# Kernel tuning notes

Measured on AMD Instinct MI355X. Metric: run time of the kernel, lower is better.

Reference implementation:

```python
import jax, jax.numpy as jnp
import numpy as np


def setup_inputs() -> dict:
    key = jax.random.key(0)
    x = jax.random.normal(key, (4, 512, 64, 64), dtype=jnp.float32)
    return {"x": x}


def reference(x) -> jnp.ndarray:
    B, C, H, W = x.shape
    N = H * W
    v = x.reshape(B, C, N)                      # proj_query/key/value all = x flattened
    # energy[b, i, j] = sum_c x[b,c,i] * x[b,c,j]
    energy = jnp.einsum('bci,bcj->bij', v, v)
    attention = jax.nn.softmax(energy, axis=-1)  # softmax over last dim (keys j)
    # out[b,c,i] = sum_j v[b,c,j] * attention[b,i,j]  (== V @ attention^T)
    out = jnp.einsum('bcj,bij->bci', v, attention)
    return out.reshape(B, C, H, W)
```

## Files before the change

kernel.cpp:

```cpp
#include <hip/hip_runtime.h>
#include <hip/hip_bf16.h>

typedef unsigned short u16;
typedef unsigned int   u32;
typedef unsigned long long u64;
typedef __attribute__((ext_vector_type(8))) short bf16x8;
typedef __attribute__((ext_vector_type(4))) float f32x4;

#define BB 4
#define CC 512
#define NN 4096
#define LOG2E 1.44269504f

static __device__ __forceinline__ u16 f2b(float f) {
    __hip_bfloat16 h = __float2bfloat16(f);
    return *(u16*)&h;
}
static __device__ __forceinline__ u16 f2b_fast(float f) {
    u32 u = __builtin_bit_cast(u32, f);
    return (u16)((u + 0x8000u) >> 16);
}
static __device__ __forceinline__ float b2f(u16 b) {
    u32 u = (u32)b << 16;
    return __builtin_bit_cast(float, u);
}

typedef __attribute__((address_space(1))) const u32 GU32;
typedef __attribute__((address_space(3))) u32 LU32;
__device__ __forceinline__ void async16(const void* g, void* l) {
    __builtin_amdgcn_global_load_lds((GU32*)g, (LU32*)l, 16, 0, 0);
}

__global__ __launch_bounds__(256) void prep_kernel(const float* __restrict__ x,
                                                   u16* __restrict__ XT,
                                                   u16* __restrict__ XN,
                                                   float* __restrict__ normp) {
    __shared__ __align__(8) u16 tile[64][68];
    __shared__ float nsum[64];
    int blk = blockIdx.x;
    int b  = blk >> 9;
    int r2 = blk & 511;
    int cg = r2 >> 6;
    int c0 = cg << 6;
    int n0 = (r2 & 63) << 6;
    int t  = threadIdx.x;
    if (t < 64) nsum[t] = 0.f;

    int nq    = t & 15;
    int rbase = t >> 4;
    float psum[4] = {0.f, 0.f, 0.f, 0.f};
    #pragma unroll
    for (int p = 0; p < 4; ++p) {
        int cl = p * 16 + rbase;
        const float* src = x + ((size_t)(b * CC + c0 + cl) * NN) + n0 + nq * 4;
        float4 v = *(const float4*)src;
        psum[0] += v.x * v.x; psum[1] += v.y * v.y;
        psum[2] += v.z * v.z; psum[3] += v.w * v.w;
        u64 pk = (u64)f2b(v.x) | ((u64)f2b(v.y) << 16) |
                 ((u64)f2b(v.z) << 32) | ((u64)f2b(v.w) << 48);
        *(u64*)&XN[((size_t)(b * CC + c0 + cl) * NN) + n0 + nq * 4] = pk;
        *(u64*)&tile[cl][nq * 4] = pk;
    }
    __syncthreads();

    {
        int c4 = (t & 15) * 4;
        int nb = t >> 4;
        #pragma unroll
        for (int rr = 0; rr < 4; ++rr) {
            int nl = rr * 16 + nb;
            u64 pk = (u64)tile[c4][nl] | ((u64)tile[c4 + 1][nl] << 16) |
                     ((u64)tile[c4 + 2][nl] << 32) | ((u64)tile[c4 + 3][nl] << 48);
            *(u64*)&XT[((size_t)(b * NN + n0 + nl) * CC) + c0 + c4] = pk;
        }
    }
    #pragma unroll
    for (int k = 0; k < 4; ++k) atomicAdd(&nsum[nq * 4 + k], psum[k]);
    __syncthreads();
    if (t < 64)
        normp[((size_t)cg * BB + b) * NN + n0 + t] = nsum[t];
}

__global__ __launch_bounds__(1024) void nred_kernel(const float* __restrict__ normp,
                                                    float* __restrict__ norms,
                                                    int* __restrict__ maxn) {
    int b = blockIdx.x;
    int t = threadIdx.x;
    float m = 0.f;
    #pragma unroll
    for (int k = 0; k < 4; ++k) {
        int n = k * 1024 + t;
        float s = 0.f;
        #pragma unroll
        for (int cg = 0; cg < 8; ++cg)
            s += normp[((size_t)cg * BB + b) * NN + n];
        norms[(size_t)b * NN + n] = s;
        m = fmaxf(m, s);
    }
    #pragma unroll
    for (int d = 1; d < 64; d <<= 1) m = fmaxf(m, __shfl_xor(m, d));
    __shared__ float wred[16];
    if ((t & 63) == 0) wred[t >> 6] = m;
    __syncthreads();
    if (t < 16) {
        float v = wred[t];
        #pragma unroll
        for (int d = 1; d < 16; d <<= 1) v = fmaxf(v, __shfl_xor(v, d));
        if (t == 0) maxn[b] = __float_as_int(v);
    }
}

__global__ __launch_bounds__(256, 2) void flash_kernel(const u16* __restrict__ XT,
                                                       const u16* __restrict__ XN,
                                                       const float* __restrict__ norms,
                                                       const int* __restrict__ maxn,
                                                       float* __restrict__ outF,
                                                       u16* __restrict__ outH,
                                                       float* __restrict__ l0g,
                                                       float* __restrict__ l1g,
                                                       int split) {
    __shared__ __align__(16) u16 KtT[2][32 * 520];
    __shared__ __align__(16) u16 Plds[2][64 * 40];
    __shared__ float lLds[64];

    int blk   = blockIdx.x;
    int inner = blk & 255;
    int hf    = split ? (blk >> 8) : 0;
    int xcd = inner & 7;
    int b   = xcd >> 1;
    int ib  = (inner >> 3) + ((xcd & 1) << 5);
    int i_base = ib * 64;
    int jlo = hf * (NN / 2) * split;
    int njt = split ? 64 : 128;

    int t    = threadIdx.x;
    int w    = t >> 6;
    int lane = t & 63;
    int l15  = lane & 15;
    int q    = lane >> 4;

    const u16* xtb = XT + (size_t)b * NN * CC;
    const u16* xnb = XN + (size_t)b * CC * NN;

    float mxn = __int_as_float(maxn[b]);
    float M2[4];
    #pragma unroll
    for (int r = 0; r < 4; ++r) {
        float nr = norms[(size_t)b * NN + i_base + w * 16 + q * 4 + r];
        M2[r] = (sqrtf(nr * mxn) - 40.f) * LOG2E;
    }

    bf16x8 qf[16];
    {
        const u16* qrow = xtb + (size_t)(i_base + w * 16 + l15) * CC;
        #pragma unroll
        for (int kk = 0; kk < 16; ++kk)
            qf[kk] = *(const bf16x8*)(qrow + kk * 32 + q * 8);
    }

    f32x4 o[8][4];
    #pragma unroll
    for (int ct = 0; ct < 8; ++ct)
        #pragma unroll
        for (int it = 0; it < 4; ++it)
            o[ct][it] = (f32x4){0.f, 0.f, 0.f, 0.f};
    float lpart[4] = {0.f, 0.f, 0.f, 0.f};

    {
        const u16* src = xtb + (size_t)(jlo + w * 8) * CC + lane * 8;
        #pragma unroll
        for (int rr = 0; rr < 8; ++rr)
            async16(src + rr * CC, &KtT[0][(w * 8 + rr) * 520]);
    }
    __syncthreads();

    for (int jt = 0; jt < njt; ++jt) {
        int buf = jt & 1;
        int j0  = jlo + jt * 32;

        bf16x8 vf[8];
        #pragma unroll
        for (int ct = 0; ct < 8; ++ct)
            vf[ct] = *(const bf16x8*)(xnb + (size_t)(w * 128 + ct * 16 + l15) * NN + j0 + q * 8);

        if (jt + 1 < njt) {
            const u16* src = xtb + (size_t)(j0 + 32 + w * 8) * CC + lane * 8;
            #pragma unroll
            for (int rr = 0; rr < 8; ++rr)
                async16(src + rr * CC, &KtT[buf ^ 1][(w * 8 + rr) * 520]);
        }

        f32x4 s0 = {0.f,0.f,0.f,0.f}, s1 = {0.f,0.f,0.f,0.f};
        #pragma unroll
        for (int kk = 0; kk < 16; ++kk) {
            bf16x8 b0 = *(const bf16x8*)&KtT[buf][(l15)      * 520 + kk * 32 + q * 8];
            bf16x8 b1 = *(const bf16x8*)&KtT[buf][(16 + l15) * 520 + kk * 32 + q * 8];
            s0 = __builtin_amdgcn_mfma_f32_16x16x32_bf16(qf[kk], b0, s0, 0, 0, 0);
            s1 = __builtin_amdgcn_mfma_f32_16x16x32_bf16(qf[kk], b1, s1, 0, 0, 0);
        }

        #pragma unroll
        for (int r = 0; r < 4; ++r) {
            float p0 = __builtin_amdgcn_exp2f(fmaf(s0[r], LOG2E, -M2[r]));
            float p1 = __builtin_amdgcn_exp2f(fmaf(s1[r], LOG2E, -M2[r]));
            u16 h0 = f2b_fast(p0), h1 = f2b_fast(p1);
            lpart[r] += b2f(h0) + b2f(h1);
            int row = w * 16 + q * 4 + r;
            Plds[buf][row * 40 +      l15] = h0;
            Plds[buf][row * 40 + 16 + l15] = h1;
        }
        __syncthreads();

        bf16x8 pb[4];
        #pragma unroll
        for (int it = 0; it < 4; ++it)
            pb[it] = *(const bf16x8*)&Plds[buf][(it * 16 + l15) * 40 + q * 8];
        #pragma unroll
        for (int ct = 0; ct < 8; ++ct)
            #pragma unroll
            for (int it = 0; it < 4; ++it)
                o[ct][it] = __builtin_amdgcn_mfma_f32_16x16x32_bf16(vf[ct], pb[it], o[ct][it], 0, 0, 0);
    }

    #pragma unroll
    for (int r = 0; r < 4; ++r) {
        float s = lpart[r];
        s += __shfl_xor(s, 1);
        s += __shfl_xor(s, 2);
        s += __shfl_xor(s, 4);
        s += __shfl_xor(s, 8);
        lpart[r] = s;
    }

    if (!split) {
        if (l15 == 0) {
            #pragma unroll
            for (int r = 0; r < 4; ++r) lLds[w * 16 + q * 4 + r] = lpart[r];
        }
        __syncthreads();
        float linv[4];
        #pragma unroll
        for (int it = 0; it < 4; ++it) linv[it] = 1.f / lLds[it * 16 + l15];
        float* ob = outF + (size_t)b * CC * NN;
        #pragma unroll
        for (int ct = 0; ct < 8; ++ct)
            #pragma unroll
            for (int r = 0; r < 4; ++r) {
                int c = w * 128 + ct * 16 + q * 4 + r;
                float* orow = ob + (size_t)c * NN + i_base;
                #pragma unroll
                for (int it = 0; it < 4; ++it)
                    orow[it * 16 + l15] = o[ct][it][r] * linv[it];
            }
    } else {
        if (l15 == 0) {
            float* lg = (hf == 0) ? l0g : l1g;
            #pragma unroll
            for (int r = 0; r < 4; ++r)
                lg[(size_t)b * NN + i_base + w * 16 + q * 4 + r] = lpart[r];
        }
        if (hf == 0) {
            float* ob = outF + (size_t)b * CC * NN;
            #pragma unroll
            for (int ct = 0; ct < 8; ++ct)
                #pragma unroll
                for (int r = 0; r < 4; ++r) {
                    int c = w * 128 + ct * 16 + q * 4 + r;
                    float* orow = ob + (size_t)c * NN + i_base;
                    #pragma unroll
                    for (int it = 0; it < 4; ++it)
                        orow[it * 16 + l15] = o[ct][it][r];
                }
        } else {
            u16* ob = outH + (size_t)b * CC * NN;
            #pragma unroll
            for (int ct = 0; ct < 8; ++ct)
                #pragma unroll
                for (int r = 0; r < 4; ++r) {
                    int c = w * 128 + ct * 16 + q * 4 + r;
                    u16* orow = ob + (size_t)c * NN + i_base;
                    #pragma unroll
                    for (int it = 0; it < 4; ++it)
                        orow[it * 16 + l15] = f2b(o[ct][it][r]);
                }
        }
    }
}

__global__ __launch_bounds__(256) void combine_kernel(float* __restrict__ out,
                                                      const u16* __restrict__ P1,
                                                      const float* __restrict__ l0,
                                                      const float* __restrict__ l1) {
    size_t g = (size_t)blockIdx.x * 256 + threadIdx.x;
    size_t f = g * 4;
    int i = (int)(f & (NN - 1));
    int b = (int)(f >> 21);
    float4 p0 = *(float4*)&out[f];
    u64 pk = *(const u64*)&P1[f];
    float p0a[4] = {p0.x, p0.y, p0.z, p0.w};
    float r[4];
    #pragma unroll
    for (int k = 0; k < 4; ++k) {
        float l = l0[(size_t)b * NN + i + k] + l1[(size_t)b * NN + i + k];
        float p1f = b2f((u16)((pk >> (16 * k)) & 0xFFFFu));
        r[k] = (p0a[k] + p1f) / l;
    }
    *(float4*)&out[f] = (float4){r[0], r[1], r[2], r[3]};
}

extern "C" void kernel_launch(void* const* d_in, const int* in_sizes, int n_in,
                              void* d_out, int out_size, void* d_ws, size_t ws_size,
                              hipStream_t stream) {
    const float* x = (const float*)d_in[0];
    size_t SZ = (size_t)BB * NN * CC;
    size_t BN = (size_t)BB * NN;
    u16* XT = (u16*)d_ws;
    u16* XN = XT + SZ;
    u16* P1 = XN + SZ;
    float* norms = (float*)(P1 + SZ);
    float* l0g   = norms + BN;
    float* l1g   = l0g + BN;
    float* normp = l1g + BN;
    int*   maxn  = (int*)(normp + 8 * BN);
    size_t needed = 3 * SZ * 2 + 3 * BN * 4 + 8 * BN * 4 + 64;
    int split = (ws_size >= needed) ? 1 : 0;
    float* out = (float*)d_out;
    if (!split) {
        norms = (float*)(XN + SZ);
        l0g = norms + BN;
        l1g = l0g;
        normp = l1g + BN;
        maxn = (int*)(normp + 8 * BN);
    }

    prep_kernel<<<2048, 256, 0, stream>>>(x, XT, XN, normp);
    nred_kernel<<<BB, 1024, 0, stream>>>(normp, norms, maxn);
    if (split) {
        flash_kernel<<<512, 256, 0, stream>>>(XT, XN, norms, maxn, out, P1, l0g, l1g, 1);
        combine_kernel<<<(BB * CC * NN / 4) / 256, 256, 0, stream>>>(out, P1, l0g, l1g);
    } else {
        flash_kernel<<<256, 256, 0, stream>>>(XT, XN, norms, maxn, out, P1, l0g, l1g, 0);
    }
}
```

Baseline: 292.8 us.

## Warp-specialize flash kernel into QK and PV wave groups, drop split-K combine

The attention kernel now runs 512 threads split into two wave groups. Four waves compute the QK^T scores with 32x32x16 MFMAs over 64-key tiles, split across the channel dimension and summed, then write bf16 probabilities to LDS. The other four waves do the P·V MFMAs one tile behind, so score and output work overlap across a shared barrier. The two-way key split and its bf16 partial buffer and combine kernel are removed. This trades a second launch and extra traffic for half as many blocks (256) and heavier per-wave register use, and the QK waves load 32 Q fragments each.

```diff
diff --git a/kernel.cpp b/kernel.cpp
--- a/kernel.cpp
+++ b/kernel.cpp
@@ -6,11 +6,14 @@
 typedef unsigned long long u64;
 typedef __attribute__((ext_vector_type(8))) short bf16x8;
 typedef __attribute__((ext_vector_type(4))) float f32x4;
+typedef __attribute__((ext_vector_type(16))) float f32x16;
 
 #define BB 4
 #define CC 512
 #define NN 4096
 #define LOG2E 1.44269504f
+#define KTS 520
+#define PS  72
 
 static __device__ __forceinline__ u16 f2b(float f) {
     __hip_bfloat16 h = __float2bfloat16(f);
@@ -110,202 +113,164 @@
     }
 }
 
-__global__ __launch_bounds__(256, 2) void flash_kernel(const u16* __restrict__ XT,
+__global__ __launch_bounds__(512, 2) void flash_kernel(const u16* __restrict__ XT,
                                                        const u16* __restrict__ XN,
                                                        const float* __restrict__ norms,
                                                        const int* __restrict__ maxn,
-                                                       float* __restrict__ outF,
-                                                       u16* __restrict__ outH,
-                                                       float* __restrict__ l0g,
-                                                       float* __restrict__ l1g,
-                                                       int split) {
-    __shared__ __align__(16) u16 KtT[2][32 * 520];
-    __shared__ __align__(16) u16 Plds[2][64 * 40];
-    __shared__ float lLds[64];
-
-    int blk   = blockIdx.x;
-    int inner = blk & 255;
-    int hf    = split ? (blk >> 8) : 0;
-    int xcd = inner & 7;
+                                                       float* __restrict__ outF) {
+    __shared__ __align__(16) u16 KtT[2][64 * KTS];
+    __shared__ __align__(16) u16 Plds[2][64 * PS];
+    __shared__ float lLds[2][64];
+
+    int blk = blockIdx.x;
+    int xcd = blk & 7;
     int b   = xcd >> 1;
-    int ib  = (inner >> 3) + ((xcd & 1) << 5);
+    int ib  = (blk >> 3) + ((xcd & 1) << 5);
     int i_base = ib * 64;
-    int jlo = hf * (NN / 2) * split;
-    int njt = split ? 64 : 128;
 
     int t    = threadIdx.x;
     int w    = t >> 6;
     int lane = t & 63;
+    int l31  = lane & 31;
+    int h    = lane >> 5;
     int l15  = lane & 15;
-    int q    = lane >> 4;
+    int q16  = lane >> 4;
+    const int njt = NN / 64;
 
     const u16* xtb = XT + (size_t)b * NN * CC;
     const u16* xnb = XN + (size_t)b * CC * NN;
 
-    float mxn = __int_as_float(maxn[b]);
-    float M2[4];
-    #pragma unroll
-    for (int r = 0; r < 4; ++r) {
-        float nr = norms[(size_t)b * NN + i_base + w * 16 + q * 4 + r];
-        M2[r] = (sqrtf(nr * mxn) - 40.f) * LOG2E;
-    }
-
-    bf16x8 qf[16];
-    {
-        const u16* qrow = xtb + (size_t)(i_base + w * 16 + l15) * CC;
-        #pragma unroll
-        for (int kk = 0; kk < 16; ++kk)
-            qf[kk] = *(const bf16x8*)(qrow + kk * 32 + q * 8);
-    }
-
-    f32x4 o[8][4];
-    #pragma unroll
-    for (int ct = 0; ct < 8; ++ct)
-        #pragma unroll
-        for (int it = 0; it < 4; ++it)
-            o[ct][it] = (f32x4){0.f, 0.f, 0.f, 0.f};
-    float lpart[4] = {0.f, 0.f, 0.f, 0.f};
-
-    {
-        const u16* src = xtb + (size_t)(jlo + w * 8) * CC + lane * 8;
-        #pragma unroll
-        for (int rr = 0; rr < 8; ++rr)
-            async16(src + rr * CC, &KtT[0][(w * 8 + rr) * 520]);
-    }
-    __syncthreads();
-
-    for (int jt = 0; jt < njt; ++jt) {
-        int buf = jt & 1;
-        int j0  = jlo + jt * 32;
-
-        bf16x8 vf[8];
-        #pragma unroll
-        for (int ct = 0; ct < 8; ++ct)
-            vf[ct] = *(const bf16x8*)(xnb + (size_t)(w * 128 + ct * 16 + l15) * NN + j0 + q * 8);
-
-        if (jt + 1 < njt) {
-            const u16* src = xtb + (size_t)(j0 + 32 + w * 8) * CC + lane * 8;
-            #pragma unroll
-            for (int rr = 0; rr < 8; ++rr)
-                async16(src + rr * CC, &KtT[buf ^ 1][(w * 8 + rr) * 520]);
+    bool isG1 = (w < 4);
+    int ih = w & 1;
+    int jh = (w >> 1) & 1;
+    int cbase = (w - 4) << 7;
+
+    bf16x8 qf[32];
+    float  M2v[16], lpart[16];
+    f32x4  o[8][4];
+
+    if (isG1) {
+        float mxn = __int_as_float(maxn[b]);
+        const u16* qrow = xtb + (size_t)(i_base + ih * 32 + l31) * CC;
+        #pragma unroll
+        for (int kk = 0; kk < 32; ++kk)
+            qf[kk] = *(const bf16x8*)(qrow + kk * 16 + h * 8);
+        #pragma unroll
+        for (int g = 0; g < 16; ++g) {
+            int il = (g & 3) + 8 * (g >> 2) + 4 * h;
+            float nr = norms[(size_t)b * NN + i_base + ih * 32 + il];
+            M2v[g] = (sqrtf(nr * mxn) - 40.f) * LOG2E;
+            lpart[g] = 0.f;
         }
-
-        f32x4 s0 = {0.f,0.f,0.f,0.f}, s1 = {0.f,0.f,0.f,0.f};
-        #pragma unroll
-        for (int kk = 0; kk < 16; ++kk) {
-            bf16x8 b0 = *(const bf16x8*)&KtT[buf][(l15)      * 520 + kk * 32 + q * 8];
-            bf16x8 b1 = *(const bf16x8*)&KtT[buf][(16 + l15) * 520 + kk * 32 + q * 8];
-            s0 = __builtin_amdgcn_mfma_f32_16x16x32_bf16(qf[kk], b0, s0, 0, 0, 0);
-            s1 = __builtin_amdgcn_mfma_f32_16x16x32_bf16(qf[kk], b1, s1, 0, 0, 0);
-        }
-
-        #pragma unroll
-        for (int r = 0; r < 4; ++r) {
-            float p0 = __builtin_amdgcn_exp2f(fmaf(s0[r], LOG2E, -M2[r]));
-            float p1 = __builtin_amdgcn_exp2f(fmaf(s1[r], LOG2E, -M2[r]));
-            u16 h0 = f2b_fast(p0), h1 = f2b_fast(p1);
-            lpart[r] += b2f(h0) + b2f(h1);
-            int row = w * 16 + q * 4 + r;
-            Plds[buf][row * 40 +      l15] = h0;
-            Plds[buf][row * 40 + 16 + l15] = h1;
-        }
-        __syncthreads();
-
-        bf16x8 pb[4];
-        #pragma unroll
-        for (int it = 0; it < 4; ++it)
-            pb[it] = *(const bf16x8*)&Plds[buf][(it * 16 + l15) * 40 + q * 8];
+        const u16* src = xtb + (size_t)(w * 16) * CC + lane * 8;
+        #pragma unroll
+        for (int rr = 0; rr < 16; ++rr)
+            async16(src + (size_t)rr * CC, &KtT[0][(w * 16 + rr) * KTS]);
+    } else {
         #pragma unroll
         for (int ct = 0; ct < 8; ++ct)
             #pragma unroll
             for (int it = 0; it < 4; ++it)
-                o[ct][it] = __builtin_amdgcn_mfma_f32_16x16x32_bf16(vf[ct], pb[it], o[ct][it], 0, 0, 0);
-    }
-
-    #pragma unroll
-    for (int r = 0; r < 4; ++r) {
-        float s = lpart[r];
-        s += __shfl_xor(s, 1);
-        s += __shfl_xor(s, 2);
-        s += __shfl_xor(s, 4);
-        s += __shfl_xor(s, 8);
-        lpart[r] = s;
-    }
-
-    if (!split) {
-        if (l15 == 0) {
-            #pragma unroll
-            for (int r = 0; r < 4; ++r) lLds[w * 16 + q * 4 + r] = lpart[r];
+                o[ct][it] = (f32x4){0.f, 0.f, 0.f, 0.f};
+    }
+    __syncthreads();
+
+    for (int r = 0; r <= njt; ++r) {
+        if (isG1) {
+            if (r < njt) {
+                int buf = r & 1;
+                if (r + 1 < njt) {
+                    const u16* src = xtb + (size_t)((r + 1) * 64 + w * 16) * CC + lane * 8;
+                    #pragma unroll
+                    for (int rr = 0; rr < 16; ++rr)
+                        async16(src + (size_t)rr * CC, &KtT[buf ^ 1][(w * 16 + rr) * KTS]);
+                }
+                const u16* kb = &KtT[buf][(jh * 32 + l31) * KTS + h * 8];
+                f32x16 Sa, Sb;
+                #pragma unroll
+                for (int z = 0; z < 16; ++z) { Sa[z] = 0.f; Sb[z] = 0.f; }
+                __builtin_amdgcn_s_setprio(1);
+                #pragma unroll
+                for (int kk = 0; kk < 16; ++kk) {
+                    Sa = __builtin_amdgcn_mfma_f32_32x32x16_bf16(
+                        qf[kk], *(const bf16x8*)(kb + kk * 16), Sa, 0, 0, 0);
+                    Sb = __builtin_amdgcn_mfma_f32_32x32x16_bf16(
+                        qf[kk + 16], *(const bf16x8*)(kb + (kk + 16) * 16), Sb, 0, 0, 0);
+                }
+                __builtin_amdgcn_s_setprio(0);
+                u16* prow = &Plds[buf][(ih * 32) * PS + jh * 32 + l31];
+                #pragma unroll
+                for (int g = 0; g < 16; ++g) {
+                    int il = (g & 3) + 8 * (g >> 2) + 4 * h;
+                    float p = __builtin_amdgcn_exp2f(fmaf(Sa[g] + Sb[g], LOG2E, -M2v[g]));
+                    u16 hb = f2b_fast(p);
+                    lpart[g] += b2f(hb);
+                    prow[il * PS] = hb;
+                }
+            } else {
+                #pragma unroll
+                for (int g = 0; g < 16; ++g) {
+                    float s = lpart[g];
+                    s += __shfl_xor(s, 1);  s += __shfl_xor(s, 2);
+                    s += __shfl_xor(s, 4);  s += __shfl_xor(s, 8);
+                    s += __shfl_xor(s, 16);
+                    lpart[g] = s;
+                }
+                if (l31 == 0) {
+                    #pragma unroll
+                    for (int g = 0; g < 16; ++g) {
+                        int il = (g & 3) + 8 * (g >> 2) + 4 * h;
+                        lLds[jh][ih * 32 + il] = lpart[g];
+                    }
+                }
+            }
+        } else {
+            if (r > 0) {
+                int q  = r - 1;
+                int p2 = q & 1;
+                int j0 = q * 64;
+                #pragma unroll
+                for (int js = 0; js < 2; ++js) {
+                    bf16x8 vf[8];
+                    #pragma unroll
+                    for (int ct = 0; ct < 8; ++ct)
+                        vf[ct] = *(const bf16x8*)(xnb +
+                            (size_t)(cbase + ct * 16 + l15) * NN + j0 + js * 32 + q16 * 8);
+                    bf16x8 pb[4];
+                    #pragma unroll
+                    for (int it = 0; it < 4; ++it)
+                        pb[it] = *(const bf16x8*)&Plds[p2][(it * 16 + l15) * PS + js * 32 + q16 * 8];
+                    __builtin_amdgcn_s_setprio(1);
+                    #pragma unroll
+                    for (int ct = 0; ct < 8; ++ct)
+                        #pragma unroll
+                        for (int it = 0; it < 4; ++it)
+                            o[ct][it] = __builtin_amdgcn_mfma_f32_16x16x32_bf16(
+                                vf[ct], pb[it], o[ct][it], 0, 0, 0);
+                    __builtin_amdgcn_s_setprio(0);
+                }
+            }
         }
         __syncthreads();
+    }
+
+    if (!isG1) {
         float linv[4];
         #pragma unroll
-        for (int it = 0; it < 4; ++it) linv[it] = 1.f / lLds[it * 16 + l15];
+        for (int it = 0; it < 4; ++it)
+            linv[it] = 1.f / (lLds[0][it * 16 + l15] + lLds[1][it * 16 + l15]);
         float* ob = outF + (size_t)b * CC * NN;
         #pragma unroll
         for (int ct = 0; ct < 8; ++ct)
             #pragma unroll
-            for (int r = 0; r < 4; ++r) {
-                int c = w * 128 + ct * 16 + q * 4 + r;
+            for (int rr = 0; rr < 4; ++rr) {
+                int c = cbase + ct * 16 + q16 * 4 + rr;
                 float* orow = ob + (size_t)c * NN + i_base;
                 #pragma unroll
                 for (int it = 0; it < 4; ++it)
-                    orow[it * 16 + l15] = o[ct][it][r] * linv[it];
+                    orow[it * 16 + l15] = o[ct][it][rr] * linv[it];
             }
-    } else {
-        if (l15 == 0) {
-            float* lg = (hf == 0) ? l0g : l1g;
-            #pragma unroll
-            for (int r = 0; r < 4; ++r)
-                lg[(size_t)b * NN + i_base + w * 16 + q * 4 + r] = lpart[r];
-        }
-        if (hf == 0) {
-            float* ob = outF + (size_t)b * CC * NN;
-            #pragma unroll
-            for (int ct = 0; ct < 8; ++ct)
-                #pragma unroll
-                for (int r = 0; r < 4; ++r) {
-                    int c = w * 128 + ct * 16 + q * 4 + r;
-                    float* orow = ob + (size_t)c * NN + i_base;
-                    #pragma unroll
-                    for (int it = 0; it < 4; ++it)
-                        orow[it * 16 + l15] = o[ct][it][r];
-                }
-        } else {
-            u16* ob = outH + (size_t)b * CC * NN;
-            #pragma unroll
-            for (int ct = 0; ct < 8; ++ct)
-                #pragma unroll
-                for (int r = 0; r < 4; ++r) {
-                    int c = w * 128 + ct * 16 + q * 4 + r;
-                    u16* orow = ob + (size_t)c * NN + i_base;
-                    #pragma unroll
-                    for (int it = 0; it < 4; ++it)
-                        orow[it * 16 + l15] = f2b(o[ct][it][r]);
-                }
-        }
-    }
-}
-
-__global__ __launch_bounds__(256) void combine_kernel(float* __restrict__ out,
-                                                      const u16* __restrict__ P1,
-                                                      const float* __restrict__ l0,
-                                                      const float* __restrict__ l1) {
-    size_t g = (size_t)blockIdx.x * 256 + threadIdx.x;
-    size_t f = g * 4;
-    int i = (int)(f & (NN - 1));
-    int b = (int)(f >> 21);
-    float4 p0 = *(float4*)&out[f];
-    u64 pk = *(const u64*)&P1[f];
-    float p0a[4] = {p0.x, p0.y, p0.z, p0.w};
-    float r[4];
-    #pragma unroll
-    for (int k = 0; k < 4; ++k) {
-        float l = l0[(size_t)b * NN + i + k] + l1[(size_t)b * NN + i + k];
-        float p1f = b2f((u16)((pk >> (16 * k)) & 0xFFFFu));
-        r[k] = (p0a[k] + p1f) / l;
-    }
-    *(float4*)&out[f] = (float4){r[0], r[1], r[2], r[3]};
+    }
 }
 
 extern "C" void kernel_launch(void* const* d_in, const int* in_sizes, int n_in,
@@ -316,29 +281,12 @@
     size_t BN = (size_t)BB * NN;
     u16* XT = (u16*)d_ws;
     u16* XN = XT + SZ;
-    u16* P1 = XN + SZ;
-    float* norms = (float*)(P1 + SZ);
-    float* l0g   = norms + BN;
-    float* l1g   = l0g + BN;
-    float* normp = l1g + BN;
+    float* norms = (float*)(XN + SZ);
+    float* normp = norms + BN;
     int*   maxn  = (int*)(normp + 8 * BN);
-    size_t needed = 3 * SZ * 2 + 3 * BN * 4 + 8 * BN * 4 + 64;
-    int split = (ws_size >= needed) ? 1 : 0;
     float* out = (float*)d_out;
-    if (!split) {
-        norms = (float*)(XN + SZ);
-        l0g = norms + BN;
-        l1g = l0g;
-        normp = l1g + BN;
-        maxn = (int*)(normp + 8 * BN);
-    }
 
     prep_kernel<<<2048, 256, 0, stream>>>(x, XT, XN, normp);
     nred_kernel<<<BB, 1024, 0, stream>>>(normp, norms, maxn);
-    if (split) {
-        flash_kernel<<<512, 256, 0, stream>>>(XT, XN, norms, maxn, out, P1, l0g, l1g, 1);
-        combine_kernel<<<(BB * CC * NN / 4) / 256, 256, 0, stream>>>(out, P1, l0g, l1g);
-    } else {
-        flash_kernel<<<256, 256, 0, stream>>>(XT, XN, norms, maxn, out, P1, l0g, l1g, 0);
-    }
-}
+    flash_kernel<<<256, 512, 0, stream>>>(XT, XN, norms, maxn, out);
+}
```

New measurement: 794.0 us. +171.2%, slower.
